# Kernel tuning notes

Hardware: AMD Instinct MI355X
Metric: run time of the kernel (lower is better)

Reference implementation:

```python
import jax, jax.numpy as jnp
import numpy as np

EPS = 1e-3  # BN1d eps from norm_cfg


def _vfe_layer(x, W, gamma, beta, max_out, cat_max):
    """x: (N, M, Cin); W: (Cout, Cin) torch Linear layout; BN in training mode
    (batch stats over voxels N and points M per channel), then ReLU."""
    y = jnp.einsum('nmc,oc->nmo', x, W)            # (N, M, Cout)
    mean = y.mean(axis=(0, 1))                     # (Cout,)
    var = y.var(axis=(0, 1))                       # biased var, as BN uses
    y = (y - mean) * jax.lax.rsqrt(var + EPS) * gamma + beta
    pointwise = jax.nn.relu(y)                     # (N, M, Cout)
    if not max_out:
        return pointwise
    aggregated = pointwise.max(axis=1, keepdims=True)  # (N, 1, Cout)
    if not cat_max:
        return aggregated[:, 0, :]                 # (N, Cout)
    M = x.shape[1]
    repeated = jnp.broadcast_to(aggregated, (x.shape[0], M, aggregated.shape[2]))
    return jnp.concatenate([pointwise, repeated], axis=2)  # (N, M, 2*Cout)


def setup_inputs() -> dict:
    key = jax.random.key(0)
    ks = jax.random.split(key, 3)
    N, M, C = 20000, 64, 10
    return {
        'voxel_feats': jax.random.normal(ks[0], (N, M, C), dtype=jnp.float32),
        'W0': jax.random.normal(ks[1], (64, C), dtype=jnp.float32) * (1.0 / np.sqrt(C)),
        'gamma0': jnp.ones((64,), dtype=jnp.float32),
        'beta0': jnp.zeros((64,), dtype=jnp.float32),
        'W1': jax.random.normal(ks[2], (128, 128), dtype=jnp.float32) * (1.0 / np.sqrt(128)),
        'gamma1': jnp.ones((128,), dtype=jnp.float32),
        'beta1': jnp.zeros((128,), dtype=jnp.float32),
    }


def reference(voxel_feats, W0, gamma0, beta0, W1, gamma1, beta1):
    # layer 0: in=10 -> out=64, max_out=True, cat_max=True -> (N, M, 128)
    x = _vfe_layer(voxel_feats, W0, gamma0, beta0, max_out=True, cat_max=True)
    # layer 1 (last): in=128 -> out=128, max_out=True, cat_max=False -> (N, 128)
    x = _vfe_layer(x, W1, gamma1, beta1, max_out=True, cat_max=False)
    return x
```

## Files before the change

### kernel.cpp

```cpp
#include <hip/hip_runtime.h>

#define NVOX 20000
#define MPTS 64
#define CIN  10
#define NM   (NVOX*MPTS)
#define EPSBN 1e-3f

#define WS_SCALE0 0
#define WS_SHIFT0 64
#define WS_SCALE1 128
#define WS_SHIFT1 256

#define NB0   512
#define P0STR 72
#define NB1   2000
#define NBF   2000

typedef short bf16x8 __attribute__((ext_vector_type(8)));
typedef float f32x4  __attribute__((ext_vector_type(4)));
typedef unsigned int u32x4 __attribute__((ext_vector_type(4)));

__device__ __forceinline__ unsigned short f2bf(float f) {
    union { float f; unsigned u; } v; v.f = f;
    unsigned r = v.u + 0x7FFFu + ((v.u >> 16) & 1u);
    return (unsigned short)(r >> 16);
}
__device__ __forceinline__ unsigned cvtpk(float lo, float hi) {
    unsigned d;
    asm("v_cvt_pk_bf16_f32 %0, %1, %2" : "=v"(d) : "v"(lo), "v"(hi));
    return d;
}
__device__ __forceinline__ unsigned pkmax(unsigned a, unsigned b) {
    unsigned d;
    asm("v_pk_max_u16 %0, %1, %2" : "=v"(d) : "v"(a), "v"(b));
    return d;
}

__global__ __launch_bounds__(256) void k_stats0(const float* __restrict__ x,
                                                float* __restrict__ p0) {
    __shared__ float sm[4][P0STR];
    float sx[CIN];
    float sxx[55];
#pragma unroll
    for (int i = 0; i < CIN; i++) sx[i] = 0.f;
#pragma unroll
    for (int k = 0; k < 55; k++) sxx[k] = 0.f;

    const int t = threadIdx.x;
    const int tid = blockIdx.x * 256 + t;

    for (int g = tid; g < NM / 2; g += NB0 * 256) {
        const float4* xp = (const float4*)(x + (size_t)g * 20);
        float4 a = xp[0], b = xp[1], c = xp[2], d = xp[3], e = xp[4];
        float v0[CIN] = {a.x, a.y, a.z, a.w, b.x, b.y, b.z, b.w, c.x, c.y};
        float v1[CIN] = {c.z, c.w, d.x, d.y, d.z, d.w, e.x, e.y, e.z, e.w};
#pragma unroll
        for (int i = 0; i < CIN; i++) sx[i] += v0[i] + v1[i];
#pragma unroll
        for (int i = 0; i < CIN; i++)
#pragma unroll
            for (int j = 0; j <= i; j++)
                sxx[i * (i + 1) / 2 + j] += v0[i] * v0[j] + v1[i] * v1[j];
    }

    const int l = t & 63, w = t >> 6;
#pragma unroll
    for (int i = 0; i < CIN; i++) {
        float v = sx[i];
#pragma unroll
        for (int off = 32; off; off >>= 1) v += __shfl_xor(v, off, 64);
        if (l == 0) sm[w][i] = v;
    }
#pragma unroll
    for (int k = 0; k < 55; k++) {
        float v = sxx[k];
#pragma unroll
        for (int off = 32; off; off >>= 1) v += __shfl_xor(v, off, 64);
        if (l == 0) sm[w][10 + k] = v;
    }
    __syncthreads();
    if (t < 65)
        p0[blockIdx.x * P0STR + t] = sm[0][t] + sm[1][t] + sm[2][t] + sm[3][t];
}

__global__ void k_finalize0(const float* __restrict__ p0, float* __restrict__ ws,
                            const float* __restrict__ w0,
                            const float* __restrict__ gamma0, const float* __restrict__ beta0) {
    __shared__ float s[P0STR];
    const int t = threadIdx.x;
    if (t < 65) {
        float acc = 0.f;
#pragma unroll 8
        for (int r = 0; r < NB0; r++) acc += p0[r * P0STR + t];
        s[t] = acc;
    }
    __syncthreads();
    if (t < 64) {
        float w[CIN];
#pragma unroll
        for (int i = 0; i < CIN; i++) w[i] = w0[t * CIN + i];
        float m = 0.f;
#pragma unroll
        for (int i = 0; i < CIN; i++) m += w[i] * s[i];
        m *= (1.f / NM);
        float q = 0.f;
#pragma unroll
        for (int i = 0; i < CIN; i++)
#pragma unroll
            for (int j = 0; j <= i; j++)
                q += ((i == j) ? 1.f : 2.f) * w[i] * w[j] * s[10 + i * (i + 1) / 2 + j];
        q *= (1.f / NM);
        float var = q - m * m;
        float scale = gamma0[t] * rsqrtf(var + EPSBN);
        ws[WS_SCALE0 + t] = scale;
        ws[WS_SHIFT0 + t] = beta0[t] - m * scale;
    }
}

__global__ void k_finalize1(const float* __restrict__ p1, float* __restrict__ ws,
                            const float* __restrict__ gamma1, const float* __restrict__ beta1) {
    __shared__ float sm[2][4];
    const int c = blockIdx.x;
    const int t = threadIdx.x, l = t & 63, w = t >> 6;
    float s = 0.f, qq = 0.f;
    for (int r = t; r < NB1; r += 256) {
        s  += p1[(size_t)r * 256 + c];
        qq += p1[(size_t)r * 256 + 128 + c];
    }
#pragma unroll
    for (int off = 32; off; off >>= 1) { s += __shfl_xor(s, off, 64); qq += __shfl_xor(qq, off, 64); }
    if (l == 0) { sm[0][w] = s; sm[1][w] = qq; }
    __syncthreads();
    if (t == 0) {
        float S = sm[0][0] + sm[0][1] + sm[0][2] + sm[0][3];
        float Q = sm[1][0] + sm[1][1] + sm[1][2] + sm[1][3];
        float m = S * (1.f / NM);
        float var = Q * (1.f / NM) - m * m;
        float scale = gamma1[c] * rsqrtf(var + EPSBN);
        ws[WS_SCALE1 + c] = scale;
        ws[WS_SHIFT1 + c] = beta1[c] - m * scale;
    }
}

template <bool STATS>
__global__ __launch_bounds__(256) void k_pass(const float* __restrict__ x,
                                              const float* __restrict__ w0,
                                              const float* __restrict__ w1,
                                              const float* __restrict__ ws,
                                              float* __restrict__ pout) {
    __shared__ unsigned short xB[MPTS * 40];
    __shared__ unsigned short zB[MPTS * 72];
    __shared__ unsigned short aggP[4 * 64];
    __shared__ float pbuf[256];

    const int t  = threadIdx.x;
    const int l  = t & 63;
    const int w  = t >> 6;
    const int lr = l & 15;
    const int lg = l >> 4;
    const int srow = 16 * w + (l >> 2);
    const int ssub = l & 3;
    const int prow = 16 * w + lr;

    for (int i = t; i < MPTS * 40 / 2; i += 256) ((unsigned*)xB)[i] = 0u;
    __syncthreads();
    if (t < 64) xB[t * 40 + 10] = 0x3F80;

    bf16x8 w0f[4];
#pragma unroll
    for (int mi = 0; mi < 4; mi++) {
        int ch = 16 * mi + lr;
        float sc = ws[WS_SCALE0 + ch], sh = ws[WS_SHIFT0 + ch];
        bf16x8 f;
#pragma unroll
        for (int j = 0; j < 8; j++) {
            int k = 8 * lg + j;
            float v = (k < CIN) ? sc * w0[ch * CIN + k] : (k == CIN ? sh : 0.f);
            f[j] = (short)f2bf(v);
        }
        w0f[mi] = f;
    }

    bf16x8 wfrag[2][4];
#pragma unroll
    for (int njl = 0; njl < 2; njl++) {
        const float* wrow = w1 + (32 * w + 16 * njl + lr) * 128;
#pragma unroll
        for (int ks = 0; ks < 4; ks++) {
            float4 a = *(const float4*)(wrow + 32 * ks + 8 * lg);
            float4 b = *(const float4*)(wrow + 32 * ks + 8 * lg + 4);
            bf16x8 f;
            f[0] = (short)f2bf(a.x); f[1] = (short)f2bf(a.y);
            f[2] = (short)f2bf(a.z); f[3] = (short)f2bf(a.w);
            f[4] = (short)f2bf(b.x); f[5] = (short)f2bf(b.y);
            f[6] = (short)f2bf(b.z); f[7] = (short)f2bf(b.w);
            wfrag[njl][ks] = f;
        }
    }

    float sc1[2], sh1[2];
    if (!STATS) {
#pragma unroll
        for (int njl = 0; njl < 2; njl++) {
            int col = 32 * w + 16 * njl + lr;
            sc1[njl] = ws[WS_SCALE1 + col];
            sh1[njl] = ws[WS_SHIFT1 + col];
        }
    }
    float as_[2] = {0.f, 0.f}, aq[2] = {0.f, 0.f};

    __syncthreads();

    float2 pfa, pfb;
    {
        const float* xr = x + (size_t)blockIdx.x * 640 + srow * 10;
        if (ssub < 2) { pfa = *(const float2*)(xr + ssub * 4); pfb = *(const float2*)(xr + ssub * 4 + 2); }
        else if (ssub == 2) { pfa = *(const float2*)(xr + 8); }
    }

    const int nblk = STATS ? NB1 : NBF;
    for (int n = blockIdx.x; n < NVOX; n += nblk) {
        if (ssub < 2) {
            uint2 d = { cvtpk(pfa.x, pfa.y), cvtpk(pfb.x, pfb.y) };
            *(uint2*)&xB[srow * 40 + ssub * 4] = d;
        } else if (ssub == 2) {
            *(unsigned*)&xB[srow * 40 + 8] = cvtpk(pfa.x, pfa.y);
        }
        {
            int nn = n + nblk;
            if (nn < NVOX) {
                const float* xr = x + (size_t)nn * 640 + srow * 10;
                if (ssub < 2) { pfa = *(const float2*)(xr + ssub * 4); pfb = *(const float2*)(xr + ssub * 4 + 2); }
                else if (ssub == 2) { pfa = *(const float2*)(xr + 8); }
            }
        }

        {
            bf16x8 bx = *(const bf16x8*)&xB[prow * 40 + 8 * lg];
#pragma unroll
            for (int mi = 0; mi < 4; mi++) {
                f32x4 zz = {0.f, 0.f, 0.f, 0.f};
                f32x4 a0 = __builtin_amdgcn_mfma_f32_16x16x32_bf16(w0f[mi], bx, zz, 0, 0, 0);
                uint2 dd = { cvtpk(fmaxf(a0[0], 0.f), fmaxf(a0[1], 0.f)),
                             cvtpk(fmaxf(a0[2], 0.f), fmaxf(a0[3], 0.f)) };
                *(uint2*)&zB[prow * 72 + 16 * mi + 4 * lg] = dd;
            }
        }

        {
            int cs = l & 7;
            int pa = 16 * w + 2 * (l >> 3);
            u32x4 ra = *(const u32x4*)&zB[pa * 72 + cs * 8];
            u32x4 rb = *(const u32x4*)&zB[(pa + 1) * 72 + cs * 8];
            u32x4 m;
#pragma unroll
            for (int k2 = 0; k2 < 4; k2++) m[k2] = pkmax(ra[k2], rb[k2]);
#pragma unroll
            for (int off = 8; off <= 32; off <<= 1)
#pragma unroll
                for (int k2 = 0; k2 < 4; k2++) m[k2] = pkmax(m[k2], __shfl_xor(m[k2], off));
            if (l < 8) *(u32x4*)&aggP[w * 64 + l * 8] = m;
        }

        asm volatile("s_waitcnt lgkmcnt(0)" ::: "memory");
        __builtin_amdgcn_s_barrier();

        bf16x8 bz[4][2];
#pragma unroll
        for (int pj = 0; pj < 4; pj++) {
            int p = 16 * pj + lr;
#pragma unroll
            for (int ks = 0; ks < 2; ks++)
                bz[pj][ks] = *(const bf16x8*)&zB[p * 72 + (4 * ks + lg) * 8];
        }
        bf16x8 gfrag[2];
#pragma unroll
        for (int ks = 0; ks < 2; ks++) {
            int sl = (4 * ks + lg) * 8;
            u32x4 g = *(const u32x4*)&aggP[sl];
#pragma unroll
            for (int wv = 1; wv < 4; wv++) {
                u32x4 h2 = *(const u32x4*)&aggP[wv * 64 + sl];
#pragma unroll
                for (int k2 = 0; k2 < 4; k2++) g[k2] = pkmax(g[k2], h2[k2]);
            }
            gfrag[ks] = __builtin_bit_cast(bf16x8, g);
        }

        asm volatile("s_waitcnt lgkmcnt(0)" ::: "memory");
        __builtin_amdgcn_s_barrier();

        f32x4 dacc[2];
#pragma unroll
        for (int njl = 0; njl < 2; njl++) {
            f32x4 zz = {0.f, 0.f, 0.f, 0.f};
            zz = __builtin_amdgcn_mfma_f32_16x16x32_bf16(gfrag[0], wfrag[njl][2], zz, 0, 0, 0);
            dacc[njl] = __builtin_amdgcn_mfma_f32_16x16x32_bf16(gfrag[1], wfrag[njl][3], zz, 0, 0, 0);
        }

        float vm[2] = {0.f, 0.f};
#pragma unroll
        for (int njl = 0; njl < 2; njl++) {
#pragma unroll
            for (int mi = 0; mi < 4; mi++) {
                f32x4 acc = dacc[njl];
                acc = __builtin_amdgcn_mfma_f32_16x16x32_bf16(bz[mi][0], wfrag[njl][0], acc, 0, 0, 0);
                acc = __builtin_amdgcn_mfma_f32_16x16x32_bf16(bz[mi][1], wfrag[njl][1], acc, 0, 0, 0);
                if (STATS) {
#pragma unroll
                    for (int r = 0; r < 4; r++) { as_[njl] += acc[r]; aq[njl] += acc[r] * acc[r]; }
                } else {
#pragma unroll
                    for (int r = 0; r < 4; r++)
                        vm[njl] = fmaxf(vm[njl], fmaxf(fmaf(acc[r], sc1[njl], sh1[njl]), 0.f));
                }
            }
        }

        if (!STATS) {
#pragma unroll
            for (int njl = 0; njl < 2; njl++) {
                float v = vm[njl];
                v = fmaxf(v, __shfl_xor(v, 16));
                v = fmaxf(v, __shfl_xor(v, 32));
                if (l < 16) pout[(size_t)n * 128 + 32 * w + 16 * njl + l] = v;
            }
        }
    }

    if (STATS) {
#pragma unroll
        for (int njl = 0; njl < 2; njl++) {
            float s = as_[njl];
            s += __shfl_xor(s, 16); s += __shfl_xor(s, 32);
            float qq = aq[njl];
            qq += __shfl_xor(qq, 16); qq += __shfl_xor(qq, 32);
            if (l < 16) {
                int col = 32 * w + 16 * njl + l;
                pbuf[col] = s;
                pbuf[128 + col] = qq;
            }
        }
        __syncthreads();
        pout[(size_t)blockIdx.x * 256 + t] = pbuf[t];
    }
}

extern "C" void kernel_launch(void* const* d_in, const int* in_sizes, int n_in,
                              void* d_out, int out_size, void* d_ws, size_t ws_size,
                              hipStream_t stream) {
    (void)in_sizes; (void)n_in; (void)out_size; (void)ws_size;
    const float* x      = (const float*)d_in[0];
    const float* W0     = (const float*)d_in[1];
    const float* gamma0 = (const float*)d_in[2];
    const float* beta0  = (const float*)d_in[3];
    const float* W1     = (const float*)d_in[4];
    const float* gamma1 = (const float*)d_in[5];
    const float* beta1  = (const float*)d_in[6];
    float* out = (float*)d_out;
    float* ws  = (float*)d_ws;

    k_stats0<<<NB0, 256, 0, stream>>>(x, out);
    k_finalize0<<<1, 256, 0, stream>>>(out, ws, W0, gamma0, beta0);
    k_pass<true><<<NB1, 256, 0, stream>>>(x, W0, W1, ws, out);
    k_finalize1<<<128, 256, 0, stream>>>(out, ws, gamma1, beta1);
    k_pass<false><<<NBF, 256, 0, stream>>>(x, W0, W1, ws, out);
}
```

Before: 220.9 us.

## Repartition layer-1 GEMM so each wave owns its points and all channels

Layer-1 GEMM work is reassigned so each wave computes all 128 output channels for its own 16 points, with the full W1 fragment set held in registers. The A fragments come straight from the wave's own z rows, so the shared xB staging buffer and one barrier per voxel are gone; x is converted to bf16 in registers, with the bias 1.0 term inserted directly. Per-voxel aggregates and output maxima are double-buffered in shared memory so the final cross-wave max and global store are deferred to the next iteration. The changes also raise the launch-bounds occupancy hint, fix the iteration count at 10 voxels per block, and double the stats0 grid; the catch is much higher register pressure (32 W1 fragments per lane), which may cause spills.

```diff
diff --git a/kernel.cpp b/kernel.cpp
--- a/kernel.cpp
+++ b/kernel.cpp
@@ -11,10 +11,10 @@
 #define WS_SCALE1 128
 #define WS_SHIFT1 256
 
-#define NB0   512
+#define NB0   1024
 #define P0STR 72
-#define NB1   2000
-#define NBF   2000
+#define NBP   2000
+#define NITER 10
 
 typedef short bf16x8 __attribute__((ext_vector_type(8)));
 typedef float f32x4  __attribute__((ext_vector_type(4)));
@@ -123,7 +123,7 @@
     const int c = blockIdx.x;
     const int t = threadIdx.x, l = t & 63, w = t >> 6;
     float s = 0.f, qq = 0.f;
-    for (int r = t; r < NB1; r += 256) {
+    for (int r = t; r < NBP; r += 256) {
         s  += p1[(size_t)r * 256 + c];
         qq += p1[(size_t)r * 256 + 128 + c];
     }
@@ -143,28 +143,22 @@
 }
 
 template <bool STATS>
-__global__ __launch_bounds__(256) void k_pass(const float* __restrict__ x,
-                                              const float* __restrict__ w0,
-                                              const float* __restrict__ w1,
-                                              const float* __restrict__ ws,
-                                              float* __restrict__ pout) {
-    __shared__ unsigned short xB[MPTS * 40];
+__global__ __launch_bounds__(256, 2) void k_pass(const float* __restrict__ x,
+                                                 const float* __restrict__ w0,
+                                                 const float* __restrict__ w1,
+                                                 const float* __restrict__ ws,
+                                                 float* __restrict__ pout) {
     __shared__ unsigned short zB[MPTS * 72];
-    __shared__ unsigned short aggP[4 * 64];
-    __shared__ float pbuf[256];
+    __shared__ unsigned short aggP[2 * 4 * 64];
+    __shared__ float vmP[2 * 4 * 132];
+    __shared__ float pbuf[4 * 256];
 
     const int t  = threadIdx.x;
     const int l  = t & 63;
     const int w  = t >> 6;
     const int lr = l & 15;
     const int lg = l >> 4;
-    const int srow = 16 * w + (l >> 2);
-    const int ssub = l & 3;
     const int prow = 16 * w + lr;
-
-    for (int i = t; i < MPTS * 40 / 2; i += 256) ((unsigned*)xB)[i] = 0u;
-    __syncthreads();
-    if (t < 64) xB[t * 40 + 10] = 0x3F80;
 
     bf16x8 w0f[4];
 #pragma unroll
@@ -181,10 +175,10 @@
         w0f[mi] = f;
     }
 
-    bf16x8 wfrag[2][4];
-#pragma unroll
-    for (int njl = 0; njl < 2; njl++) {
-        const float* wrow = w1 + (32 * w + 16 * njl + lr) * 128;
+    bf16x8 wfrag[8][4];
+#pragma unroll
+    for (int njl = 0; njl < 8; njl++) {
+        const float* wrow = w1 + (16 * njl + lr) * 128;
 #pragma unroll
         for (int ks = 0; ks < 4; ks++) {
             float4 a = *(const float4*)(wrow + 32 * ks + 8 * lg);
@@ -198,54 +192,67 @@
         }
     }
 
-    float sc1[2], sh1[2];
+    float sc1[8], sh1[8];
     if (!STATS) {
 #pragma unroll
-        for (int njl = 0; njl < 2; njl++) {
-            int col = 32 * w + 16 * njl + lr;
+        for (int njl = 0; njl < 8; njl++) {
+            int col = 16 * njl + lr;
             sc1[njl] = ws[WS_SCALE1 + col];
             sh1[njl] = ws[WS_SHIFT1 + col];
         }
     }
-    float as_[2] = {0.f, 0.f}, aq[2] = {0.f, 0.f};
-
-    __syncthreads();
-
-    float2 pfa, pfb;
+    float as_[8], aq[8];
+    if (STATS) {
+#pragma unroll
+        for (int njl = 0; njl < 8; njl++) { as_[njl] = 0.f; aq[njl] = 0.f; }
+    }
+
+    float2 pfA, pfB, pfC, pfD;
     {
-        const float* xr = x + (size_t)blockIdx.x * 640 + srow * 10;
-        if (ssub < 2) { pfa = *(const float2*)(xr + ssub * 4); pfb = *(const float2*)(xr + ssub * 4 + 2); }
-        else if (ssub == 2) { pfa = *(const float2*)(xr + 8); }
-    }
-
-    const int nblk = STATS ? NB1 : NBF;
-    for (int n = blockIdx.x; n < NVOX; n += nblk) {
-        if (ssub < 2) {
-            uint2 d = { cvtpk(pfa.x, pfa.y), cvtpk(pfb.x, pfb.y) };
-            *(uint2*)&xB[srow * 40 + ssub * 4] = d;
-        } else if (ssub == 2) {
-            *(unsigned*)&xB[srow * 40 + 8] = cvtpk(pfa.x, pfa.y);
-        }
-        {
-            int nn = n + nblk;
-            if (nn < NVOX) {
-                const float* xr = x + (size_t)nn * 640 + srow * 10;
-                if (ssub < 2) { pfa = *(const float2*)(xr + ssub * 4); pfb = *(const float2*)(xr + ssub * 4 + 2); }
-                else if (ssub == 2) { pfa = *(const float2*)(xr + 8); }
-            }
-        }
-
-        {
-            bf16x8 bx = *(const bf16x8*)&xB[prow * 40 + 8 * lg];
-#pragma unroll
-            for (int mi = 0; mi < 4; mi++) {
-                f32x4 zz = {0.f, 0.f, 0.f, 0.f};
-                f32x4 a0 = __builtin_amdgcn_mfma_f32_16x16x32_bf16(w0f[mi], bx, zz, 0, 0, 0);
-                uint2 dd = { cvtpk(fmaxf(a0[0], 0.f), fmaxf(a0[1], 0.f)),
-                             cvtpk(fmaxf(a0[2], 0.f), fmaxf(a0[3], 0.f)) };
-                *(uint2*)&zB[prow * 72 + 16 * mi + 4 * lg] = dd;
-            }
-        }
+        const float* xr = x + (size_t)blockIdx.x * 640 + prow * CIN;
+        if (lg == 0) {
+            pfA = *(const float2*)(xr + 0); pfB = *(const float2*)(xr + 2);
+            pfC = *(const float2*)(xr + 4); pfD = *(const float2*)(xr + 6);
+        } else if (lg == 1) {
+            pfA = *(const float2*)(xr + 8);
+        }
+    }
+
+    for (int k = 0; k < NITER; k++) {
+        const int n = blockIdx.x + k * NBP;
+        const int buf = k & 1;
+
+        u32x4 bxu = {0u, 0u, 0u, 0u};
+        if (lg == 0) {
+            bxu[0] = cvtpk(pfA.x, pfA.y); bxu[1] = cvtpk(pfB.x, pfB.y);
+            bxu[2] = cvtpk(pfC.x, pfC.y); bxu[3] = cvtpk(pfD.x, pfD.y);
+        } else if (lg == 1) {
+            bxu[0] = cvtpk(pfA.x, pfA.y);
+            bxu[1] = 0x00003F80u;
+        }
+        bf16x8 bx = __builtin_bit_cast(bf16x8, bxu);
+
+        if (k < NITER - 1) {
+            const float* xr = x + (size_t)(n + NBP) * 640 + prow * CIN;
+            if (lg == 0) {
+                pfA = *(const float2*)(xr + 0); pfB = *(const float2*)(xr + 2);
+                pfC = *(const float2*)(xr + 4); pfD = *(const float2*)(xr + 6);
+            } else if (lg == 1) {
+                pfA = *(const float2*)(xr + 8);
+            }
+        }
+
+#pragma unroll
+        for (int mi = 0; mi < 4; mi++) {
+            f32x4 zz = {0.f, 0.f, 0.f, 0.f};
+            f32x4 a0 = __builtin_amdgcn_mfma_f32_16x16x32_bf16(w0f[mi], bx, zz, 0, 0, 0);
+            uint2 dd = { cvtpk(fmaxf(a0[0], 0.f), fmaxf(a0[1], 0.f)),
+                         cvtpk(fmaxf(a0[2], 0.f), fmaxf(a0[3], 0.f)) };
+            *(uint2*)&zB[prow * 72 + 16 * mi + 4 * lg] = dd;
+        }
+
+        bf16x8 af0 = *(const bf16x8*)&zB[prow * 72 + 8 * lg];
+        bf16x8 af1 = *(const bf16x8*)&zB[prow * 72 + 32 + 8 * lg];
 
         {
             int cs = l & 7;
@@ -259,90 +266,90 @@
             for (int off = 8; off <= 32; off <<= 1)
 #pragma unroll
                 for (int k2 = 0; k2 < 4; k2++) m[k2] = pkmax(m[k2], __shfl_xor(m[k2], off));
-            if (l < 8) *(u32x4*)&aggP[w * 64 + l * 8] = m;
+            if (l < 8) *(u32x4*)&aggP[(buf * 4 + w) * 64 + l * 8] = m;
         }
 
         asm volatile("s_waitcnt lgkmcnt(0)" ::: "memory");
         __builtin_amdgcn_s_barrier();
 
-        bf16x8 bz[4][2];
-#pragma unroll
-        for (int pj = 0; pj < 4; pj++) {
-            int p = 16 * pj + lr;
-#pragma unroll
-            for (int ks = 0; ks < 2; ks++)
-                bz[pj][ks] = *(const bf16x8*)&zB[p * 72 + (4 * ks + lg) * 8];
-        }
-        bf16x8 gfrag[2];
+        if (!STATS && k > 0) {
+            if (l < 32) {
+                int pb = buf ^ 1;
+                int o = 32 * w + l;
+                float v0 = vmP[(pb * 4 + 0) * 132 + o];
+                float v1 = vmP[(pb * 4 + 1) * 132 + o];
+                float v2 = vmP[(pb * 4 + 2) * 132 + o];
+                float v3 = vmP[(pb * 4 + 3) * 132 + o];
+                pout[(size_t)(n - NBP) * 128 + o] = fmaxf(fmaxf(v0, v1), fmaxf(v2, v3));
+            }
+        }
+
+        bf16x8 gf[2];
 #pragma unroll
         for (int ks = 0; ks < 2; ks++) {
             int sl = (4 * ks + lg) * 8;
-            u32x4 g = *(const u32x4*)&aggP[sl];
+            u32x4 g = *(const u32x4*)&aggP[(buf * 4 + 0) * 64 + sl];
 #pragma unroll
             for (int wv = 1; wv < 4; wv++) {
-                u32x4 h2 = *(const u32x4*)&aggP[wv * 64 + sl];
+                u32x4 h2 = *(const u32x4*)&aggP[(buf * 4 + wv) * 64 + sl];
 #pragma unroll
                 for (int k2 = 0; k2 < 4; k2++) g[k2] = pkmax(g[k2], h2[k2]);
             }
-            gfrag[ks] = __builtin_bit_cast(bf16x8, g);
-        }
-
+            gf[ks] = __builtin_bit_cast(bf16x8, g);
+        }
+
+#pragma unroll
+        for (int njl = 0; njl < 8; njl++) {
+            f32x4 acc = {0.f, 0.f, 0.f, 0.f};
+            acc = __builtin_amdgcn_mfma_f32_16x16x32_bf16(af0, wfrag[njl][0], acc, 0, 0, 0);
+            acc = __builtin_amdgcn_mfma_f32_16x16x32_bf16(af1, wfrag[njl][1], acc, 0, 0, 0);
+            acc = __builtin_amdgcn_mfma_f32_16x16x32_bf16(gf[0], wfrag[njl][2], acc, 0, 0, 0);
+            acc = __builtin_amdgcn_mfma_f32_16x16x32_bf16(gf[1], wfrag[njl][3], acc, 0, 0, 0);
+            if (STATS) {
+                as_[njl] += (acc[0] + acc[1]) + (acc[2] + acc[3]);
+                aq[njl]  += (acc[0] * acc[0] + acc[1] * acc[1]) +
+                            (acc[2] * acc[2] + acc[3] * acc[3]);
+            } else {
+                float v0 = fmaxf(fmaf(acc[0], sc1[njl], sh1[njl]), 0.f);
+                float v1 = fmaxf(fmaf(acc[1], sc1[njl], sh1[njl]), 0.f);
+                float v2 = fmaxf(fmaf(acc[2], sc1[njl], sh1[njl]), 0.f);
+                float v3 = fmaxf(fmaf(acc[3], sc1[njl], sh1[njl]), 0.f);
+                float m = fmaxf(fmaxf(v0, v1), fmaxf(v2, v3));
+                m = fmaxf(m, __shfl_xor(m, 16));
+                m = fmaxf(m, __shfl_xor(m, 32));
+                if (l < 16) vmP[(buf * 4 + w) * 132 + njl * 16 + lr] = m;
+            }
+        }
+    }
+
+    if (!STATS) {
         asm volatile("s_waitcnt lgkmcnt(0)" ::: "memory");
         __builtin_amdgcn_s_barrier();
-
-        f32x4 dacc[2];
-#pragma unroll
-        for (int njl = 0; njl < 2; njl++) {
-            f32x4 zz = {0.f, 0.f, 0.f, 0.f};
-            zz = __builtin_amdgcn_mfma_f32_16x16x32_bf16(gfrag[0], wfrag[njl][2], zz, 0, 0, 0);
-            dacc[njl] = __builtin_amdgcn_mfma_f32_16x16x32_bf16(gfrag[1], wfrag[njl][3], zz, 0, 0, 0);
-        }
-
-        float vm[2] = {0.f, 0.f};
-#pragma unroll
-        for (int njl = 0; njl < 2; njl++) {
-#pragma unroll
-            for (int mi = 0; mi < 4; mi++) {
-                f32x4 acc = dacc[njl];
-                acc = __builtin_amdgcn_mfma_f32_16x16x32_bf16(bz[mi][0], wfrag[njl][0], acc, 0, 0, 0);
-                acc = __builtin_amdgcn_mfma_f32_16x16x32_bf16(bz[mi][1], wfrag[njl][1], acc, 0, 0, 0);
-                if (STATS) {
-#pragma unroll
-                    for (int r = 0; r < 4; r++) { as_[njl] += acc[r]; aq[njl] += acc[r] * acc[r]; }
-                } else {
-#pragma unroll
-                    for (int r = 0; r < 4; r++)
-                        vm[njl] = fmaxf(vm[njl], fmaxf(fmaf(acc[r], sc1[njl], sh1[njl]), 0.f));
-                }
-            }
-        }
-
-        if (!STATS) {
-#pragma unroll
-            for (int njl = 0; njl < 2; njl++) {
-                float v = vm[njl];
-                v = fmaxf(v, __shfl_xor(v, 16));
-                v = fmaxf(v, __shfl_xor(v, 32));
-                if (l < 16) pout[(size_t)n * 128 + 32 * w + 16 * njl + l] = v;
-            }
-        }
-    }
-
-    if (STATS) {
-#pragma unroll
-        for (int njl = 0; njl < 2; njl++) {
+        if (l < 32) {
+            int pb = (NITER - 1) & 1;
+            int o = 32 * w + l;
+            int n = blockIdx.x + (NITER - 1) * NBP;
+            float v0 = vmP[(pb * 4 + 0) * 132 + o];
+            float v1 = vmP[(pb * 4 + 1) * 132 + o];
+            float v2 = vmP[(pb * 4 + 2) * 132 + o];
+            float v3 = vmP[(pb * 4 + 3) * 132 + o];
+            pout[(size_t)n * 128 + o] = fmaxf(fmaxf(v0, v1), fmaxf(v2, v3));
+        }
+    } else {
+#pragma unroll
+        for (int njl = 0; njl < 8; njl++) {
             float s = as_[njl];
             s += __shfl_xor(s, 16); s += __shfl_xor(s, 32);
-            float qq = aq[njl];
-            qq += __shfl_xor(qq, 16); qq += __shfl_xor(qq, 32);
+            float qv = aq[njl];
+            qv += __shfl_xor(qv, 16); qv += __shfl_xor(qv, 32);
             if (l < 16) {
-                int col = 32 * w + 16 * njl + l;
-                pbuf[col] = s;
-                pbuf[128 + col] = qq;
+                pbuf[w * 256 + njl * 16 + lr] = s;
+                pbuf[w * 256 + 128 + njl * 16 + lr] = qv;
             }
         }
         __syncthreads();
-        pout[(size_t)blockIdx.x * 256 + t] = pbuf[t];
+        float tot = pbuf[t] + pbuf[256 + t] + pbuf[512 + t] + pbuf[768 + t];
+        pout[(size_t)blockIdx.x * 256 + t] = tot;
     }
 }
 
@@ -362,7 +369,7 @@
 
     k_stats0<<<NB0, 256, 0, stream>>>(x, out);
     k_finalize0<<<1, 256, 0, stream>>>(out, ws, W0, gamma0, beta0);
-    k_pass<true><<<NB1, 256, 0, stream>>>(x, W0, W1, ws, out);
+    k_pass<true><<<NBP, 256, 0, stream>>>(x, W0, W1, ws, out);
     k_finalize1<<<128, 256, 0, stream>>>(out, ws, gamma1, beta1);
-    k_pass<false><<<NBF, 256, 0, stream>>>(x, W0, W1, ws, out);
-}
+    k_pass<false><<<NBP, 256, 0, stream>>>(x, W0, W1, ws, out);
+}
```

New measurement: 505.3 us. +128.7%, slower.

## Process two voxels per iteration with double-buffered LDS and register-built input fragments

Applied to the files above, without the earlier changes.

The fused pass kernel now handles two voxels per loop iteration with double-buffered shared-memory buffers, so each iteration needs one barrier instead of two. Input point features are loaded straight into registers and packed into the bf16 MFMA fragment, with the bias-one column inserted in registers, which removes the xB staging buffer and its store/load. The loop is fixed at NITER=5, which assumes NVOX equals 2*NBP*NITER. NB0 is also doubled for the stats kernel. Shared-memory use grows, and the unrolled two-voxel body may raise register pressure.

```diff
diff --git a/kernel.cpp b/kernel.cpp
--- a/kernel.cpp
+++ b/kernel.cpp
@@ -11,10 +11,10 @@
 #define WS_SCALE1 128
 #define WS_SHIFT1 256
 
-#define NB0   512
+#define NB0   1024
 #define P0STR 72
-#define NB1   2000
-#define NBF   2000
+#define NBP   2000
+#define NITER 5
 
 typedef short bf16x8 __attribute__((ext_vector_type(8)));
 typedef float f32x4  __attribute__((ext_vector_type(4)));
@@ -123,7 +123,7 @@
     const int c = blockIdx.x;
     const int t = threadIdx.x, l = t & 63, w = t >> 6;
     float s = 0.f, qq = 0.f;
-    for (int r = t; r < NB1; r += 256) {
+    for (int r = t; r < NBP; r += 256) {
         s  += p1[(size_t)r * 256 + c];
         qq += p1[(size_t)r * 256 + 128 + c];
     }
@@ -148,9 +148,8 @@
                                               const float* __restrict__ w1,
                                               const float* __restrict__ ws,
                                               float* __restrict__ pout) {
-    __shared__ unsigned short xB[MPTS * 40];
-    __shared__ unsigned short zB[MPTS * 72];
-    __shared__ unsigned short aggP[4 * 64];
+    __shared__ unsigned short zB[2][2][MPTS * 72];
+    __shared__ unsigned short aggP[2][2][4 * 64];
     __shared__ float pbuf[256];
 
     const int t  = threadIdx.x;
@@ -158,13 +157,7 @@
     const int w  = t >> 6;
     const int lr = l & 15;
     const int lg = l >> 4;
-    const int srow = 16 * w + (l >> 2);
-    const int ssub = l & 3;
     const int prow = 16 * w + lr;
-
-    for (int i = t; i < MPTS * 40 / 2; i += 256) ((unsigned*)xB)[i] = 0u;
-    __syncthreads();
-    if (t < 64) xB[t * 40 + 10] = 0x3F80;
 
     bf16x8 w0f[4];
 #pragma unroll
@@ -209,98 +202,80 @@
     }
     float as_[2] = {0.f, 0.f}, aq[2] = {0.f, 0.f};
 
-    __syncthreads();
-
-    float2 pfa, pfb;
-    {
-        const float* xr = x + (size_t)blockIdx.x * 640 + srow * 10;
-        if (ssub < 2) { pfa = *(const float2*)(xr + ssub * 4); pfb = *(const float2*)(xr + ssub * 4 + 2); }
-        else if (ssub == 2) { pfa = *(const float2*)(xr + 8); }
-    }
-
-    const int nblk = STATS ? NB1 : NBF;
-    for (int n = blockIdx.x; n < NVOX; n += nblk) {
-        if (ssub < 2) {
-            uint2 d = { cvtpk(pfa.x, pfa.y), cvtpk(pfb.x, pfb.y) };
-            *(uint2*)&xB[srow * 40 + ssub * 4] = d;
-        } else if (ssub == 2) {
-            *(unsigned*)&xB[srow * 40 + 8] = cvtpk(pfa.x, pfa.y);
-        }
-        {
-            int nn = n + nblk;
-            if (nn < NVOX) {
-                const float* xr = x + (size_t)nn * 640 + srow * 10;
-                if (ssub < 2) { pfa = *(const float2*)(xr + ssub * 4); pfb = *(const float2*)(xr + ssub * 4 + 2); }
-                else if (ssub == 2) { pfa = *(const float2*)(xr + 8); }
-            }
-        }
-
-        {
-            bf16x8 bx = *(const bf16x8*)&xB[prow * 40 + 8 * lg];
-#pragma unroll
-            for (int mi = 0; mi < 4; mi++) {
-                f32x4 zz = {0.f, 0.f, 0.f, 0.f};
-                f32x4 a0 = __builtin_amdgcn_mfma_f32_16x16x32_bf16(w0f[mi], bx, zz, 0, 0, 0);
-                uint2 dd = { cvtpk(fmaxf(a0[0], 0.f), fmaxf(a0[1], 0.f)),
-                             cvtpk(fmaxf(a0[2], 0.f), fmaxf(a0[3], 0.f)) };
-                *(uint2*)&zB[prow * 72 + 16 * mi + 4 * lg] = dd;
-            }
-        }
-
-        {
-            int cs = l & 7;
-            int pa = 16 * w + 2 * (l >> 3);
-            u32x4 ra = *(const u32x4*)&zB[pa * 72 + cs * 8];
-            u32x4 rb = *(const u32x4*)&zB[(pa + 1) * 72 + cs * 8];
-            u32x4 m;
-#pragma unroll
-            for (int k2 = 0; k2 < 4; k2++) m[k2] = pkmax(ra[k2], rb[k2]);
-#pragma unroll
-            for (int off = 8; off <= 32; off <<= 1)
-#pragma unroll
-                for (int k2 = 0; k2 < 4; k2++) m[k2] = pkmax(m[k2], __shfl_xor(m[k2], off));
-            if (l < 8) *(u32x4*)&aggP[w * 64 + l * 8] = m;
-        }
-
-        asm volatile("s_waitcnt lgkmcnt(0)" ::: "memory");
-        __builtin_amdgcn_s_barrier();
-
+    auto PF = [&](int n, float2& r0, float2& r1, float2& r2, float2& r3) {
+        const float* xr = x + (size_t)n * 640 + prow * CIN;
+        if (lg == 0) {
+            r0 = *(const float2*)(xr + 0); r1 = *(const float2*)(xr + 2);
+            r2 = *(const float2*)(xr + 4); r3 = *(const float2*)(xr + 6);
+        } else if (lg == 1) {
+            r0 = *(const float2*)(xr + 8);
+        }
+    };
+    auto MKBX = [&](float2 r0, float2 r1, float2 r2, float2 r3) -> bf16x8 {
+        u32x4 u = {0u, 0u, 0u, 0u};
+        if (lg == 0) {
+            u[0] = cvtpk(r0.x, r0.y); u[1] = cvtpk(r1.x, r1.y);
+            u[2] = cvtpk(r2.x, r2.y); u[3] = cvtpk(r3.x, r3.y);
+        } else if (lg == 1) {
+            u[0] = cvtpk(r0.x, r0.y);
+            u[1] = 0x00003F80u;
+        }
+        return __builtin_bit_cast(bf16x8, u);
+    };
+    auto L0 = [&](bf16x8 bx, int buf, int s) {
+#pragma unroll
+        for (int mi = 0; mi < 4; mi++) {
+            f32x4 zz = {0.f, 0.f, 0.f, 0.f};
+            f32x4 a0 = __builtin_amdgcn_mfma_f32_16x16x32_bf16(w0f[mi], bx, zz, 0, 0, 0);
+            uint2 dd = { cvtpk(fmaxf(a0[0], 0.f), fmaxf(a0[1], 0.f)),
+                         cvtpk(fmaxf(a0[2], 0.f), fmaxf(a0[3], 0.f)) };
+            *(uint2*)&zB[buf][s][prow * 72 + 16 * mi + 4 * lg] = dd;
+        }
+    };
+    auto AGG = [&](int buf, int s) {
+        int cs = l & 7;
+        int pa = 16 * w + 2 * (l >> 3);
+        u32x4 ra = *(const u32x4*)&zB[buf][s][pa * 72 + cs * 8];
+        u32x4 rb = *(const u32x4*)&zB[buf][s][(pa + 1) * 72 + cs * 8];
+        u32x4 m;
+#pragma unroll
+        for (int k2 = 0; k2 < 4; k2++) m[k2] = pkmax(ra[k2], rb[k2]);
+#pragma unroll
+        for (int off = 8; off <= 32; off <<= 1)
+#pragma unroll
+            for (int k2 = 0; k2 < 4; k2++) m[k2] = pkmax(m[k2], __shfl_xor(m[k2], off));
+        if (l < 8) *(u32x4*)&aggP[buf][s][w * 64 + l * 8] = m;
+    };
+    auto CONSUME = [&](int buf, int s, int n) {
         bf16x8 bz[4][2];
 #pragma unroll
-        for (int pj = 0; pj < 4; pj++) {
-            int p = 16 * pj + lr;
+        for (int pj = 0; pj < 4; pj++)
 #pragma unroll
             for (int ks = 0; ks < 2; ks++)
-                bz[pj][ks] = *(const bf16x8*)&zB[p * 72 + (4 * ks + lg) * 8];
-        }
-        bf16x8 gfrag[2];
+                bz[pj][ks] = *(const bf16x8*)&zB[buf][s][(16 * pj + lr) * 72 + (4 * ks + lg) * 8];
+        bf16x8 gf[2];
 #pragma unroll
         for (int ks = 0; ks < 2; ks++) {
             int sl = (4 * ks + lg) * 8;
-            u32x4 g = *(const u32x4*)&aggP[sl];
+            u32x4 g = *(const u32x4*)&aggP[buf][s][sl];
 #pragma unroll
             for (int wv = 1; wv < 4; wv++) {
-                u32x4 h2 = *(const u32x4*)&aggP[wv * 64 + sl];
+                u32x4 h2 = *(const u32x4*)&aggP[buf][s][wv * 64 + sl];
 #pragma unroll
                 for (int k2 = 0; k2 < 4; k2++) g[k2] = pkmax(g[k2], h2[k2]);
             }
-            gfrag[ks] = __builtin_bit_cast(bf16x8, g);
-        }
-
-        asm volatile("s_waitcnt lgkmcnt(0)" ::: "memory");
-        __builtin_amdgcn_s_barrier();
-
+            gf[ks] = __builtin_bit_cast(bf16x8, g);
+        }
         f32x4 dacc[2];
 #pragma unroll
         for (int njl = 0; njl < 2; njl++) {
             f32x4 zz = {0.f, 0.f, 0.f, 0.f};
-            zz = __builtin_amdgcn_mfma_f32_16x16x32_bf16(gfrag[0], wfrag[njl][2], zz, 0, 0, 0);
-            dacc[njl] = __builtin_amdgcn_mfma_f32_16x16x32_bf16(gfrag[1], wfrag[njl][3], zz, 0, 0, 0);
-        }
-
-        float vm[2] = {0.f, 0.f};
+            zz = __builtin_amdgcn_mfma_f32_16x16x32_bf16(gf[0], wfrag[njl][2], zz, 0, 0, 0);
+            dacc[njl] = __builtin_amdgcn_mfma_f32_16x16x32_bf16(gf[1], wfrag[njl][3], zz, 0, 0, 0);
+        }
 #pragma unroll
         for (int njl = 0; njl < 2; njl++) {
+            float vm = 0.f;
 #pragma unroll
             for (int mi = 0; mi < 4; mi++) {
                 f32x4 acc = dacc[njl];
@@ -312,20 +287,43 @@
                 } else {
 #pragma unroll
                     for (int r = 0; r < 4; r++)
-                        vm[njl] = fmaxf(vm[njl], fmaxf(fmaf(acc[r], sc1[njl], sh1[njl]), 0.f));
+                        vm = fmaxf(vm, fmaxf(fmaf(acc[r], sc1[njl], sh1[njl]), 0.f));
                 }
             }
-        }
-
-        if (!STATS) {
-#pragma unroll
-            for (int njl = 0; njl < 2; njl++) {
-                float v = vm[njl];
-                v = fmaxf(v, __shfl_xor(v, 16));
-                v = fmaxf(v, __shfl_xor(v, 32));
-                if (l < 16) pout[(size_t)n * 128 + 32 * w + 16 * njl + l] = v;
+            if (!STATS) {
+                vm = fmaxf(vm, __shfl_xor(vm, 16));
+                vm = fmaxf(vm, __shfl_xor(vm, 32));
+                if (l < 16) pout[(size_t)n * 128 + 32 * w + 16 * njl + l] = vm;
             }
         }
+    };
+
+    float2 aA0, aA1, aA2, aA3, aB0, aB1, aB2, aB3;
+    PF(blockIdx.x, aA0, aA1, aA2, aA3);
+    PF(blockIdx.x + NBP, aB0, aB1, aB2, aB3);
+
+    for (int k = 0; k < NITER; k++) {
+        const int buf = k & 1;
+        const int nA = blockIdx.x + k * 2 * NBP;
+        const int nB = nA + NBP;
+
+        bf16x8 bxA = MKBX(aA0, aA1, aA2, aA3);
+        bf16x8 bxB = MKBX(aB0, aB1, aB2, aB3);
+        if (k < NITER - 1) {
+            PF(nA + 2 * NBP, aA0, aA1, aA2, aA3);
+            PF(nB + 2 * NBP, aB0, aB1, aB2, aB3);
+        }
+
+        L0(bxA, buf, 0);
+        L0(bxB, buf, 1);
+        AGG(buf, 0);
+        AGG(buf, 1);
+
+        asm volatile("s_waitcnt lgkmcnt(0)" ::: "memory");
+        __builtin_amdgcn_s_barrier();
+
+        CONSUME(buf, 0, nA);
+        CONSUME(buf, 1, nB);
     }
 
     if (STATS) {
@@ -362,7 +360,7 @@
 
     k_stats0<<<NB0, 256, 0, stream>>>(x, out);
     k_finalize0<<<1, 256, 0, stream>>>(out, ws, W0, gamma0, beta0);
-    k_pass<true><<<NB1, 256, 0, stream>>>(x, W0, W1, ws, out);
+    k_pass<true><<<NBP, 256, 0, stream>>>(x, W0, W1, ws, out);
     k_finalize1<<<128, 256, 0, stream>>>(out, ws, gamma1, beta1);
-    k_pass<false><<<NBF, 256, 0, stream>>>(x, W0, W1, ws, out);
-}
+    k_pass<false><<<NBP, 256, 0, stream>>>(x, W0, W1, ws, out);
+}
```

After: 250.1 us. 13.2% more time.
